# Optimization experiments

Hardware: AMD Instinct MI355X
Metric: run time of the kernel (lower is better)

## Reference

```python
import jax, jax.numpy as jnp
import numpy as np

K = 3          # kernel_size
EPS = 1e-5     # BatchNorm eps


def setup_inputs() -> dict:
    key = jax.random.key(0)
    k1, k2, k3 = jax.random.split(key, 3)
    n, C, H, W = 8, 64, 128, 128
    x = jax.random.normal(k1, (n, C, H, W), dtype=jnp.float32)
    conv_w = jax.random.normal(k2, (C * K * K, C), dtype=jnp.float32) * np.sqrt(2.0 / (C * K * K))
    bn_gamma = jnp.ones((C * K * K,), dtype=jnp.float32)
    bn_beta = jnp.zeros((C * K * K,), dtype=jnp.float32)
    bn_mean = jnp.zeros((C * K * K,), dtype=jnp.float32)
    bn_var = jax.random.uniform(k3, (C * K * K,), dtype=jnp.float32)
    return {"x": x, "conv_w": conv_w, "bn_gamma": bn_gamma, "bn_beta": bn_beta,
            "bn_mean": bn_mean, "bn_var": bn_var}


def reference(x, conv_w, bn_gamma, bn_beta, bn_mean, bn_var):
    n, C, H, W = x.shape
    # ---- per-image dynamic filter: GAP -> 1x1 conv -> BN (eval) -> softmax over k^2 ----
    f = x.mean(axis=(2, 3))                       # (n, C)
    f = f @ conv_w.T                              # (n, C*9)  (1x1 conv on 1x1 map, no bias)
    f = (f - bn_mean) * (bn_gamma / jnp.sqrt(bn_var + EPS)) + bn_beta
    f = jax.nn.softmax(f.reshape(n, C, K * K), axis=-1)   # softmax over kernel positions
    # ---- reflect-pad + unfold (im2col), row-major kernel offsets matching F.unfold ----
    xp = jnp.pad(x, ((0, 0), (0, 0), (1, 1), (1, 1)), mode="reflect")
    patches = jnp.stack([xp[:, :, i:i + H, j:j + W]
                         for i in range(K) for j in range(K)], axis=2)  # (n, C, 9, H, W)
    # ---- softmax-weighted dynamic sum over the 9 taps ----
    out = jnp.einsum("nckhw,nck->nchw", patches, f)
    return out, x - out
```

## Files before the change

### kernel.cpp

```cpp
#include <hip/hip_runtime.h>

#define WW 128
#define HWSZ 16384
#define CC 64
#define NPLANE 512
#define NCHW 8388608
#define BN_EPS 1e-5f

__global__ __launch_bounds__(256) void dc_mean_kernel(const float* __restrict__ x,
                                                      float* __restrict__ means) {
    const int plane = blockIdx.x;
    const float4* xp = (const float4*)(x + (size_t)plane * HWSZ);
    float s = 0.f;
#pragma unroll
    for (int i = 0; i < 16; ++i) {
        float4 v = xp[threadIdx.x + i * 256];
        s += v.x + v.y + v.z + v.w;
    }
    for (int off = 32; off > 0; off >>= 1)
        s += __shfl_down(s, off, 64);
    __shared__ float wsum[4];
    if ((threadIdx.x & 63) == 0) wsum[threadIdx.x >> 6] = s;
    __syncthreads();
    if (threadIdx.x == 0)
        means[plane] = (wsum[0] + wsum[1] + wsum[2] + wsum[3]) * (1.0f / 16384.0f);
}

__global__ __launch_bounds__(256) void dc_conv_kernel(const float* __restrict__ x,
                                                      const float* __restrict__ means,
                                                      const float* __restrict__ conv_w,
                                                      const float* __restrict__ gamma,
                                                      const float* __restrict__ beta,
                                                      const float* __restrict__ bn_mean,
                                                      const float* __restrict__ bn_var,
                                                      float* __restrict__ out) {
    const int plane = blockIdx.x >> 4;
    const int rb    = blockIdx.x & 15;
    const int tid   = threadIdx.x;
    const int n = plane >> 6;
    const int c = plane & 63;

    __shared__ float sm[CC];
    __shared__ float lv[9];
    __shared__ float sw9[9];
    if (tid < CC) sm[tid] = means[n * CC + tid];
    __syncthreads();
    if (tid < 9) {
        const int j = c * 9 + tid;
        const float4* wr = (const float4*)(conv_w + j * CC);
        float dot = 0.f;
#pragma unroll
        for (int q = 0; q < 16; ++q) {
            float4 wv = wr[q];
            dot += sm[q * 4 + 0] * wv.x + sm[q * 4 + 1] * wv.y
                 + sm[q * 4 + 2] * wv.z + sm[q * 4 + 3] * wv.w;
        }
        const float g = gamma[j] * rsqrtf(bn_var[j] + BN_EPS);
        lv[tid] = (dot - bn_mean[j]) * g + beta[j];
    }
    __syncthreads();
    if (tid < 9) {
        float m = lv[0];
#pragma unroll
        for (int t = 1; t < 9; ++t) m = fmaxf(m, lv[t]);
        float den = 0.f;
#pragma unroll
        for (int t = 0; t < 9; ++t) den += __expf(lv[t] - m);
        sw9[tid] = __expf(lv[tid] - m) / den;
    }
    __syncthreads();

    float w9[9];
#pragma unroll
    for (int t = 0; t < 9; ++t) w9[t] = sw9[t];

    const int r  = tid >> 5;
    const int q  = tid & 31;
    const int h  = rb * 8 + r;
    const int w0 = q * 4;

    const float* xpl = x + (size_t)plane * HWSZ;
    const int hm = (h == 0)   ? 1   : h - 1;
    const int hp = (h == 127) ? 126 : h + 1;
    const int rows[3] = {hm, h, hp};

    float V[3][6];
#pragma unroll
    for (int ri = 0; ri < 3; ++ri) {
        const float* rowp = xpl + rows[ri] * WW;
        float4 c4 = *(const float4*)(rowp + w0);
        V[ri][1] = c4.x; V[ri][2] = c4.y; V[ri][3] = c4.z; V[ri][4] = c4.w;
        V[ri][0] = (w0 == 0)   ? rowp[1]   : rowp[w0 - 1];
        V[ri][5] = (w0 == 124) ? rowp[126] : rowp[w0 + 4];
    }

    float o[4];
#pragma unroll
    for (int p = 0; p < 4; ++p) {
        float acc = 0.f;
#pragma unroll
        for (int ri = 0; ri < 3; ++ri)
#pragma unroll
            for (int t = 0; t < 3; ++t)
                acc = fmaf(w9[ri * 3 + t], V[ri][p + t], acc);
        o[p] = acc;
    }

    const size_t base = (size_t)plane * HWSZ + (size_t)h * WW + w0;
    float4 ov = {o[0], o[1], o[2], o[3]};
    *(float4*)(out + base) = ov;
    float4 dv = {V[1][1] - o[0], V[1][2] - o[1], V[1][3] - o[2], V[1][4] - o[3]};
    *(float4*)(out + NCHW + base) = dv;
}

extern "C" void kernel_launch(void* const* d_in, const int* in_sizes, int n_in,
                              void* d_out, int out_size, void* d_ws, size_t ws_size,
                              hipStream_t stream) {
    const float* x       = (const float*)d_in[0];
    const float* conv_w  = (const float*)d_in[1];
    const float* gamma   = (const float*)d_in[2];
    const float* beta    = (const float*)d_in[3];
    const float* bn_mean = (const float*)d_in[4];
    const float* bn_var  = (const float*)d_in[5];
    float* out = (float*)d_out;
    float* means = (float*)d_ws;

    dc_mean_kernel<<<NPLANE, 256, 0, stream>>>(x, means);
    dc_conv_kernel<<<NPLANE * 16, 256, 0, stream>>>(x, means, conv_w, gamma, beta,
                                                    bn_mean, bn_var, out);
}
```

Before: 120.0 us.

## Process 32-row bands per block and parallelize the filter dot product

```diff
diff --git a/kernel.cpp b/kernel.cpp
--- a/kernel.cpp
+++ b/kernel.cpp
@@ -34,83 +34,85 @@
                                                       const float* __restrict__ bn_mean,
                                                       const float* __restrict__ bn_var,
                                                       float* __restrict__ out) {
-    const int plane = blockIdx.x >> 4;
-    const int rb    = blockIdx.x & 15;
+    const int plane = blockIdx.x >> 2;
+    const int band  = blockIdx.x & 3;
     const int tid   = threadIdx.x;
     const int n = plane >> 6;
     const int c = plane & 63;
 
-    __shared__ float sm[CC];
     __shared__ float lv[9];
-    __shared__ float sw9[9];
-    if (tid < CC) sm[tid] = means[n * CC + tid];
-    __syncthreads();
-    if (tid < 9) {
-        const int j = c * 9 + tid;
-        const float4* wr = (const float4*)(conv_w + j * CC);
-        float dot = 0.f;
-#pragma unroll
-        for (int q = 0; q < 16; ++q) {
-            float4 wv = wr[q];
-            dot += sm[q * 4 + 0] * wv.x + sm[q * 4 + 1] * wv.y
-                 + sm[q * 4 + 2] * wv.z + sm[q * 4 + 3] * wv.w;
+    if (tid < 144) {
+        const int j    = tid >> 4;
+        const int part = tid & 15;
+        const int jj = c * 9 + j;
+        float4 mv = *(const float4*)(means + n * CC + part * 4);
+        float4 wv = *(const float4*)(conv_w + (size_t)jj * CC + part * 4);
+        float d = mv.x * wv.x + mv.y * wv.y + mv.z * wv.z + mv.w * wv.w;
+        d += __shfl_down(d, 8, 16);
+        d += __shfl_down(d, 4, 16);
+        d += __shfl_down(d, 2, 16);
+        d += __shfl_down(d, 1, 16);
+        if (part == 0) {
+            const float g = gamma[jj] * rsqrtf(bn_var[jj] + BN_EPS);
+            lv[j] = (d - bn_mean[jj]) * g + beta[jj];
         }
-        const float g = gamma[j] * rsqrtf(bn_var[j] + BN_EPS);
-        lv[tid] = (dot - bn_mean[j]) * g + beta[j];
     }
     __syncthreads();
-    if (tid < 9) {
+
+    float w9[9];
+    {
         float m = lv[0];
 #pragma unroll
         for (int t = 1; t < 9; ++t) m = fmaxf(m, lv[t]);
         float den = 0.f;
+        float e[9];
 #pragma unroll
-        for (int t = 0; t < 9; ++t) den += __expf(lv[t] - m);
-        sw9[tid] = __expf(lv[tid] - m) / den;
+        for (int t = 0; t < 9; ++t) { e[t] = __expf(lv[t] - m); den += e[t]; }
+        const float inv = 1.0f / den;
+#pragma unroll
+        for (int t = 0; t < 9; ++t) w9[t] = e[t] * inv;
     }
-    __syncthreads();
-
-    float w9[9];
-#pragma unroll
-    for (int t = 0; t < 9; ++t) w9[t] = sw9[t];
 
     const int r  = tid >> 5;
     const int q  = tid & 31;
-    const int h  = rb * 8 + r;
     const int w0 = q * 4;
+    const float* xpl = x + (size_t)plane * HWSZ;
 
-    const float* xpl = x + (size_t)plane * HWSZ;
-    const int hm = (h == 0)   ? 1   : h - 1;
-    const int hp = (h == 127) ? 126 : h + 1;
-    const int rows[3] = {hm, h, hp};
+#pragma unroll
+    for (int it = 0; it < 4; ++it) {
+        const int h  = band * 32 + it * 8 + r;
+        const int hm = (h == 0)   ? 1   : h - 1;
+        const int hp = (h == 127) ? 126 : h + 1;
+        const int rows[3] = {hm, h, hp};
 
-    float V[3][6];
+        float V[3][6];
 #pragma unroll
-    for (int ri = 0; ri < 3; ++ri) {
-        const float* rowp = xpl + rows[ri] * WW;
-        float4 c4 = *(const float4*)(rowp + w0);
-        V[ri][1] = c4.x; V[ri][2] = c4.y; V[ri][3] = c4.z; V[ri][4] = c4.w;
-        V[ri][0] = (w0 == 0)   ? rowp[1]   : rowp[w0 - 1];
-        V[ri][5] = (w0 == 124) ? rowp[126] : rowp[w0 + 4];
+        for (int ri = 0; ri < 3; ++ri) {
+            const float* rowp = xpl + rows[ri] * WW;
+            float4 c4 = *(const float4*)(rowp + w0);
+            V[ri][1] = c4.x; V[ri][2] = c4.y; V[ri][3] = c4.z; V[ri][4] = c4.w;
+            V[ri][0] = (w0 == 0)   ? c4.y : rowp[w0 - 1];
+            V[ri][5] = (w0 == 124) ? c4.z : rowp[w0 + 4];
+        }
+
+        float o[4];
+#pragma unroll
+        for (int p = 0; p < 4; ++p) {
+            float acc = 0.f;
+#pragma unroll
+            for (int ri = 0; ri < 3; ++ri)
+#pragma unroll
+                for (int t = 0; t < 3; ++t)
+                    acc = fmaf(w9[ri * 3 + t], V[ri][p + t], acc);
+            o[p] = acc;
+        }
+
+        const size_t base = (size_t)plane * HWSZ + (size_t)h * WW + w0;
+        float4 ov = {o[0], o[1], o[2], o[3]};
+        *(float4*)(out + base) = ov;
+        float4 dv = {V[1][1] - o[0], V[1][2] - o[1], V[1][3] - o[2], V[1][4] - o[3]};
+        *(float4*)(out + NCHW + base) = dv;
     }
-
-    float o[4];
-#pragma unroll
-    for (int p = 0; p < 4; ++p) {
-        float acc = 0.f;
-#pragma unroll
-        for (int ri = 0; ri < 3; ++ri)
-#pragma unroll
-            for (int t = 0; t < 3; ++t)
-                acc = fmaf(w9[ri * 3 + t], V[ri][p + t], acc);
-        o[p] = acc;
-    }
-
-    const size_t base = (size_t)plane * HWSZ + (size_t)h * WW + w0;
-    float4 ov = {o[0], o[1], o[2], o[3]};
-    *(float4*)(out + base) = ov;
-    float4 dv = {V[1][1] - o[0], V[1][2] - o[1], V[1][3] - o[2], V[1][4] - o[3]};
-    *(float4*)(out + NCHW + base) = dv;
 }
 
 extern "C" void kernel_launch(void* const* d_in, const int* in_sizes, int n_in,
@@ -126,6 +128,6 @@
     float* means = (float*)d_ws;
 
     dc_mean_kernel<<<NPLANE, 256, 0, stream>>>(x, means);
-    dc_conv_kernel<<<NPLANE * 16, 256, 0, stream>>>(x, means, conv_w, gamma, beta,
-                                                    bn_mean, bn_var, out);
+    dc_conv_kernel<<<NPLANE * 4, 256, 0, stream>>>(x, means, conv_w, gamma, beta,
+                                                   bn_mean, bn_var, out);
 }
```

After: 113.7 us. 5.2% less time.
